# Kernel tuning notes

Hardware: AMD Instinct MI355X
Metric: run time of the kernel (lower is better)

## Reference

```python
import jax, jax.numpy as jnp
import numpy as np

B = 32768   # batch
T = 10      # n_track
NW = 3      # n_waypoints
D = 128     # d_model
H = 8       # num_heads
HD = D // H # head_dim = 16


def _ln(x, g, b, eps=1e-5):
    m = jnp.mean(x, axis=-1, keepdims=True)
    v = jnp.mean((x - m) ** 2, axis=-1, keepdims=True)
    return (x - m) * jax.lax.rsqrt(v + eps) * g + b


def setup_inputs() -> dict:
    key = jax.random.key(0)
    ks = jax.random.split(key, 16)
    rn = lambda k, shape, s=0.05: jax.random.normal(k, shape, dtype=jnp.float32) * s
    return {
        "track_left": jax.random.normal(ks[0], (B, T, 2), dtype=jnp.float32),
        "track_right": jax.random.normal(ks[1], (B, T, 2), dtype=jnp.float32),
        "coord_w": rn(ks[2], (D, 2), 0.5), "coord_b": jnp.zeros((D,), jnp.float32),
        "pos_emb": rn(ks[3], (T, D), 0.02),
        "side_emb": rn(ks[4], (2, D), 0.02),
        "query_emb": rn(ks[5], (NW, D), 0.02),
        "tokens_ln_g": jnp.ones((D,), jnp.float32), "tokens_ln_b": jnp.zeros((D,), jnp.float32),
        "queries_ln_g": jnp.ones((D,), jnp.float32), "queries_ln_b": jnp.zeros((D,), jnp.float32),
        "in_proj_w": rn(ks[6], (3 * D, D)), "in_proj_b": jnp.zeros((3 * D,), jnp.float32),
        "out_proj_w": rn(ks[7], (D, D)), "out_proj_b": jnp.zeros((D,), jnp.float32),
        "fc1_w": rn(ks[8], (2 * D, D)), "fc1_b": jnp.zeros((2 * D,), jnp.float32),
        "fc2_w": rn(ks[9], (D, 2 * D)), "fc2_b": jnp.zeros((D,), jnp.float32),
        "post_attn_ln_g": jnp.ones((D,), jnp.float32), "post_attn_ln_b": jnp.zeros((D,), jnp.float32),
        "post_ffn_ln_g": jnp.ones((D,), jnp.float32), "post_ffn_ln_b": jnp.zeros((D,), jnp.float32),
        "head_w": rn(ks[10], (2, D)), "head_b": jnp.zeros((2,), jnp.float32),
    }


def reference(track_left, track_right, coord_w, coord_b, pos_emb, side_emb,
              query_emb, tokens_ln_g, tokens_ln_b, queries_ln_g, queries_ln_b,
              in_proj_w, in_proj_b, out_proj_w, out_proj_b, fc1_w, fc1_b,
              fc2_w, fc2_b, post_attn_ln_g, post_attn_ln_b, post_ffn_ln_g,
              post_ffn_ln_b, head_w, head_b):
    # --- tokens: embed + add pos/side + LN ---  (dropout = eval-mode identity)
    coords = jnp.concatenate([track_left, track_right], axis=1)       # [B, 2T, 2]
    coord_feat = coords @ coord_w.T + coord_b                          # [B, 2T, D]
    pos_vecs = jnp.concatenate([pos_emb, pos_emb], axis=0)             # [2T, D]
    side_vecs = jnp.concatenate([
        jnp.broadcast_to(side_emb[0], (T, D)),
        jnp.broadcast_to(side_emb[1], (T, D))], axis=0)                # [2T, D]
    tokens = _ln(coord_feat + pos_vecs + side_vecs, tokens_ln_g, tokens_ln_b)  # [B, 2T, D]

    # --- queries (shared across batch) ---
    queries = _ln(query_emb, queries_ln_g, queries_ln_b)               # [NW, D]

    # --- MHA (batch_first, packed qkv in_proj as in nn.MultiheadAttention) ---
    wq, wk, wv = in_proj_w[:D], in_proj_w[D:2 * D], in_proj_w[2 * D:]
    bq, bk, bv = in_proj_b[:D], in_proj_b[D:2 * D], in_proj_b[2 * D:]
    q = (queries @ wq.T + bq).reshape(NW, H, HD)                       # [NW, H, HD]
    k = (tokens @ wk.T + bk).reshape(-1, 2 * T, H, HD)                 # [B, 2T, H, HD]
    v = (tokens @ wv.T + bv).reshape(-1, 2 * T, H, HD)                 # [B, 2T, H, HD]
    scores = jnp.einsum('whd,bkhd->bhwk', q, k) / jnp.sqrt(jnp.float32(HD))
    attn = jax.nn.softmax(scores, axis=-1)                             # [B, H, NW, 2T]
    ctx = jnp.einsum('bhwk,bkhd->bwhd', attn, v).reshape(-1, NW, D)    # [B, NW, D]
    attn_out = ctx @ out_proj_w.T + out_proj_b                         # [B, NW, D]

    # --- residual + LN + FFN + residual + LN + head ---
    x = _ln(queries[None, :, :] + attn_out, post_attn_ln_g, post_attn_ln_b)
    h = jax.nn.relu(x @ fc1_w.T + fc1_b)
    h = h @ fc2_w.T + fc2_b
    x = _ln(x + h, post_ffn_ln_g, post_ffn_ln_b)
    return x @ head_w.T + head_b                                       # [B, NW, 2]
```

## Files before the change

### kernel.cpp

```cpp
#include <hip/hip_runtime.h>
#include <hip/hip_bf16.h>


typedef __bf16 bf16x8 __attribute__((ext_vector_type(8)));
typedef float  f32x4  __attribute__((ext_vector_type(4)));
static_assert(sizeof(bf16x8) == 16, "bf16x8 must be 16B");

__device__ __forceinline__ unsigned short f2b(float x) {
  __bf16 h = (__bf16)x;
  return __builtin_bit_cast(unsigned short, h);
}
__device__ __forceinline__ float b2f(unsigned short u) {
  return (float)__builtin_bit_cast(__bf16, u);
}
__device__ __forceinline__ float dot4(float4 a, float4 b) {
  return a.x*b.x + a.y*b.y + a.z*b.z + a.w*b.w;
}
__device__ __forceinline__ f32x4 mfma16(bf16x8 a, bf16x8 b, f32x4 c) {
  return __builtin_amdgcn_mfma_f32_16x16x32_bf16(a, b, c, 0, 0, 0);
}

#define WS_OM    0
#define WS_FC1   49152
#define WS_FC2   114688
#define WS_QN    192000
#define WS_SB    193536
#define WS_SU    195456
#define WS_SCAL  195744
#define WS_SUB   195756
#define WS_SWB   195836
#define WS_SBB   195916

__device__ float mean128(float v, volatile float* red) {
  #pragma unroll
  for (int o = 32; o; o >>= 1) v += __shfl_down(v, o, 64);
  __syncthreads();
  if ((threadIdx.x & 63) == 0) red[threadIdx.x >> 6] = v;
  __syncthreads();
  return (red[0] + red[1]) * (1.0f / 128.0f);
}

__global__ void k_prep(
    const float* __restrict__ coord_w, const float* __restrict__ coord_b,
    const float* __restrict__ pos_emb, const float* __restrict__ side_emb,
    const float* __restrict__ query_emb,
    const float* __restrict__ tln_g, const float* __restrict__ tln_b,
    const float* __restrict__ qln_g, const float* __restrict__ qln_b,
    const float* __restrict__ ipw, const float* __restrict__ ipb,
    const float* __restrict__ opw, const float* __restrict__ opb,
    const float* __restrict__ f1w, const float* __restrict__ f2w,
    char* __restrict__ ws)
{
  const int b = blockIdx.x, tid = threadIdx.x;
  if (b >= 21) {
    if (b < 37) {
      unsigned short* dst = (unsigned short*)(ws + WS_FC1);
      int i0 = (b - 21)*2048;
      #pragma unroll
      for (int j = 0; j < 16; j++) { int i = i0 + j*128 + tid; dst[i] = f2b(f1w[i]); }
    } else {
      unsigned short* dst = (unsigned short*)(ws + WS_FC2);
      int i0 = (b - 37)*2048;
      #pragma unroll
      for (int j = 0; j < 16; j++) { int i = i0 + j*128 + tid; dst[i] = f2b(f2w[i]); }
    }
    return;
  }

  __shared__ float red[2];
  __shared__ float qn[3][128];
  __shared__ float qmat[3][128];
  __shared__ float vecA[128];
  __shared__ float vecB[128];
  __shared__ float vecC[128];
  __shared__ float kuA[128];
  __shared__ float kwA[128];
  __shared__ float kcA[128];
  const int d = tid;
  const int t = b;

  float u  = coord_w[d*2+0];
  float w2 = coord_w[d*2+1];
  float g  = tln_g[d];
  float mu = mean128(u,  red);
  float mw = mean128(w2, red);
  float uh = u - mu, wh = w2 - mw;

  #pragma unroll
  for (int w = 0; w < 3; w++) {
    float qe = query_emb[w*128 + d];
    float m  = mean128(qe, red);
    float m2 = mean128(qe*qe, red);
    float var = m2 - m*m;
    qn[w][d] = (qe - m) * rsqrtf(var + 1e-5f) * qln_g[d] + qln_b[d];
  }
  __syncthreads();
  {
    const float* wqr = ipw + d*128;
    float a0 = 0, a1 = 0, a2 = 0;
    for (int k4 = 0; k4 < 32; k4++) {
      float4 wv4 = *(const float4*)&wqr[k4*4];
      a0 += dot4(wv4, *(const float4*)&qn[0][k4*4]);
      a1 += dot4(wv4, *(const float4*)&qn[1][k4*4]);
      a2 += dot4(wv4, *(const float4*)&qn[2][k4*4]);
    }
    float bq = ipb[d];
    qmat[0][d] = a0 + bq; qmat[1][d] = a1 + bq; qmat[2][d] = a2 + bq;
  }
  __syncthreads();

  if (t < 20) {
    float base = coord_b[d] + pos_emb[(t % 10)*128 + d] + side_emb[(t < 10 ? 0 : 1)*128 + d];
    float mb = mean128(base, red);
    float bh = base - mb;
    float sub = mean128(uh*bh, red);
    float swb = mean128(wh*bh, red);
    float sbb = mean128(bh*bh, red);
    if (d == 0) {
      ((float*)(ws + WS_SUB))[t] = sub;
      ((float*)(ws + WS_SWB))[t] = swb;
      ((float*)(ws + WS_SBB))[t] = sbb;
    }
    vecA[d] = bh * g;
    __syncthreads();
    const float* wkr = ipw + (128 + d)*128;
    const float* wvr = ipw + (256 + d)*128;
    float kb = 0, vb = 0;
    for (int k4 = 0; k4 < 32; k4++) {
      float4 a4 = *(const float4*)&vecA[k4*4];
      kb += dot4(*(const float4*)&wkr[k4*4], a4);
      vb += dot4(*(const float4*)&wvr[k4*4], a4);
    }
    kuA[d] = kb;
    vecB[d] = vb;
    __syncthreads();
    if (d < 24) {
      int w = d / 8, h = d % 8;
      float s = 0;
      #pragma unroll
      for (int dl = 0; dl < 16; dl++) s += qmat[w][h*16 + dl] * kuA[h*16 + dl];
      ((float*)(ws + WS_SB))[(w*8 + h)*20 + t] = 0.25f * s;
    }
    {
      const float* opr = opw + d*128;
      float acc[8] = {0,0,0,0,0,0,0,0};
      #pragma unroll
      for (int k4 = 0; k4 < 32; k4++) {
        float4 o4 = *(const float4*)&opr[k4*4];
        acc[k4 >> 2] += dot4(o4, *(const float4*)&vecB[k4*4]);
      }
      unsigned short* OMr = (unsigned short*)(ws + WS_OM) + d*192;
      #pragma unroll
      for (int h = 0; h < 8; h++) OMr[h*20 + t] = f2b(acc[h]);
    }
  } else {
    float suu = mean128(uh*uh, red);
    float sww = mean128(wh*wh, red);
    float suw = mean128(uh*wh, red);
    if (d == 0) {
      float* sc = (float*)(ws + WS_SCAL);
      sc[0] = suu; sc[1] = sww; sc[2] = suw;
    }
    vecA[d] = uh * g; vecB[d] = wh * g; vecC[d] = tln_b[d];
    __syncthreads();
    const float* wkr = ipw + (128 + d)*128;
    const float* wvr = ipw + (256 + d)*128;
    float ku = 0, kw = 0, kc = 0, vu = 0, vw = 0, vc = 0;
    for (int k4 = 0; k4 < 32; k4++) {
      float4 a4 = *(const float4*)&vecA[k4*4];
      float4 b4 = *(const float4*)&vecB[k4*4];
      float4 c4 = *(const float4*)&vecC[k4*4];
      float4 kv = *(const float4*)&wkr[k4*4];
      float4 vv = *(const float4*)&wvr[k4*4];
      ku += dot4(kv, a4); kw += dot4(kv, b4); kc += dot4(kv, c4);
      vu += dot4(vv, a4); vw += dot4(vv, b4); vc += dot4(vv, c4);
    }
    kc += ipb[128 + d]; vc += ipb[256 + d];
    kuA[d] = ku; kwA[d] = kw; kcA[d] = kc;
    float* qnw = (float*)(ws + WS_QN);
    qnw[0*128 + d] = qn[0][d]; qnw[1*128 + d] = qn[1][d]; qnw[2*128 + d] = qn[2][d];
    __syncthreads();
    vecA[d] = vu; vecB[d] = vw; vecC[d] = vc;
    __syncthreads();
    if (d < 24) {
      int w = d / 8, h = d % 8;
      float su = 0, sw = 0, sc2 = 0;
      #pragma unroll
      for (int dl = 0; dl < 16; dl++) {
        float q = qmat[w][h*16 + dl];
        su  += q * kuA[h*16 + dl];
        sw  += q * kwA[h*16 + dl];
        sc2 += q * kcA[h*16 + dl];
      }
      float* o = (float*)(ws + WS_SU);
      o[ 0 + w*8 + h] = 0.25f * su;
      o[24 + w*8 + h] = 0.25f * sw;
      o[48 + w*8 + h] = 0.25f * sc2;
    }
    {
      const float* opr = opw + d*128;
      float au[8] = {0,0,0,0,0,0,0,0};
      float aw[8] = {0,0,0,0,0,0,0,0};
      float ac = 0;
      #pragma unroll
      for (int k4 = 0; k4 < 32; k4++) {
        float4 o4 = *(const float4*)&opr[k4*4];
        au[k4 >> 2] += dot4(o4, *(const float4*)&vecA[k4*4]);
        aw[k4 >> 2] += dot4(o4, *(const float4*)&vecB[k4*4]);
        ac          += dot4(o4, *(const float4*)&vecC[k4*4]);
      }
      unsigned short* OMr = (unsigned short*)(ws + WS_OM) + d*192;
      #pragma unroll
      for (int h = 0; h < 8; h++) {
        OMr[160 + h] = f2b(au[h]);
        OMr[168 + h] = f2b(aw[h]);
      }
      OMr[176] = f2b(ac + opb[d]);
      #pragma unroll
      for (int i = 177; i < 192; i++) OMr[i] = 0;
    }
  }
}

#define GE 16
#define MR 48
#define SMEM_SZ 32256

__global__ __launch_bounds__(256, 3) void k_main(
    const float* __restrict__ tl, const float* __restrict__ tr,
    const float* __restrict__ f1b, const float* __restrict__ f2b_,
    const float* __restrict__ pag, const float* __restrict__ pab,
    const float* __restrict__ pfg, const float* __restrict__ pfb,
    const float* __restrict__ hw, const float* __restrict__ hb,
    const char* __restrict__ ws, float* __restrict__ out)
{
  __shared__ __align__(16) char smem[SMEM_SZ];
  unsigned short* Z  = (unsigned short*)(smem);
  unsigned short* X  = (unsigned short*)(smem);
  float* Pp2  = (float*)(smem + 13056);
  float* msc2 = (float*)(smem + 14592);
  float* Op   = (float*)(smem + 14976);
  float* xr   = (float*)(smem + 19200);
  float* yr   = (float*)(smem + 20480);
  float* rsA  = (float*)(smem + 21760);
  float* Sbl  = (float*)(smem + 23040);
  float* SulA = (float*)(smem + 24960);
  float* QNl  = (float*)(smem + 25248);
  float* pagl = (float*)(smem + 26784);
  float* pabl = (float*)(smem + 27296);
  float* Pp   = (float*)(smem + 27808);
  float* mscA = (float*)(smem + 29344);
  unsigned short* h1 = (unsigned short*)(smem + 19200);

  const unsigned short* OM = (const unsigned short*)(ws + WS_OM);
  const unsigned short* W1 = (const unsigned short*)(ws + WS_FC1);
  const unsigned short* W2 = (const unsigned short*)(ws + WS_FC2);
  const float* QNw  = (const float*)(ws + WS_QN);
  const float* SBw  = (const float*)(ws + WS_SB);
  const float* SUw  = (const float*)(ws + WS_SU);
  const float* SCAL = (const float*)(ws + WS_SCAL);
  const float* SUB  = (const float*)(ws + WS_SUB);
  const float* SWB  = (const float*)(ws + WS_SWB);
  const float* SBB  = (const float*)(ws + WS_SBB);

  const int tid  = threadIdx.x;
  const int wg   = blockIdx.x;
  const int lane = tid & 63;
  const int wv   = tid >> 6;
  const int c    = lane & 15;
  const int g    = lane >> 4;
  const int nb   = wv * 32;

  for (int i = tid; i < 480; i += 256) Sbl[i] = SBw[i];
  if (tid < 72) SulA[tid] = SUw[tid];
  for (int i = tid; i < 384; i += 256) QNl[i] = QNw[i];
  if (tid < 128) { pagl[tid] = pag[tid]; pabl[tid] = pab[tid]; }
  if (tid < 48) {
    unsigned short* Zr = Z + tid*200;
    Zr[176] = 0x3F80;
    #pragma unroll
    for (int i = 177; i < 192; i++) Zr[i] = 0;
  }
  if (tid < 160) {
    int half = tid / 80;
    int i4   = tid % 80;
    const float* src = half ? tr : tl;
    float4 v = *(const float4*)(src + wg*(GE*20) + i4*4);
    int e  = i4 / 5;
    int j  = (i4 % 5) * 4;
    int t0 = half*10 + j/2;
    xr[e*20 + t0]     = v.x; yr[e*20 + t0]     = v.y;
    xr[e*20 + t0 + 1] = v.z; yr[e*20 + t0 + 1] = v.w;
  }
  __syncthreads();

  {
    float suu = SCAL[0], sww = SCAL[1], suw = SCAL[2];
    for (int i = tid; i < GE*20; i += 256) {
      int t = i % 20;
      float x = xr[i], y = yr[i];
      float var = suu*x*x + sww*y*y + 2.0f*suw*x*y
                + 2.0f*SUB[t]*x + 2.0f*SWB[t]*y + SBB[t];
      float rv = rsqrtf(var + 1e-5f);
      rsA[i] = rv; xr[i] = x*rv; yr[i] = y*rv;
    }
  }
  __syncthreads();

  if (tid < 128) {
    int e = tid >> 3, h = tid & 7;
    float xa[20], ya[20], ra[20];
    #pragma unroll
    for (int tb = 0; tb < 5; tb++) {
      float4 xv = *(const float4*)&xr[e*20 + tb*4];
      float4 yv = *(const float4*)&yr[e*20 + tb*4];
      float4 rv = *(const float4*)&rsA[e*20 + tb*4];
      xa[tb*4+0]=xv.x; xa[tb*4+1]=xv.y; xa[tb*4+2]=xv.z; xa[tb*4+3]=xv.w;
      ya[tb*4+0]=yv.x; ya[tb*4+1]=yv.y; ya[tb*4+2]=yv.z; ya[tb*4+3]=yv.w;
      ra[tb*4+0]=rv.x; ra[tb*4+1]=rv.y; ra[tb*4+2]=rv.z; ra[tb*4+3]=rv.w;
    }
    float s[3][20];
    #pragma unroll
    for (int w = 0; w < 3; w++) {
      float suv = SulA[w*8 + h], swv = SulA[24 + w*8 + h], scv = SulA[48 + w*8 + h];
      const float* sb = &Sbl[(w*8 + h)*20];
      #pragma unroll
      for (int tb = 0; tb < 5; tb++) {
        float4 s4 = *(const float4*)&sb[tb*4];
        s[w][tb*4+0] = fmaf(xa[tb*4+0],suv, fmaf(ya[tb*4+0],swv, fmaf(ra[tb*4+0],s4.x, scv)));
        s[w][tb*4+1] = fmaf(xa[tb*4+1],suv, fmaf(ya[tb*4+1],swv, fmaf(ra[tb*4+1],s4.y, scv)));
        s[w][tb*4+2] = fmaf(xa[tb*4+2],suv, fmaf(ya[tb*4+2],swv, fmaf(ra[tb*4+2],s4.z, scv)));
        s[w][tb*4+3] = fmaf(xa[tb*4+3],suv, fmaf(ya[tb*4+3],swv, fmaf(ra[tb*4+3],s4.w, scv)));
      }
    }
    unsigned short* Zr0 = Z + e*3*200;
    #pragma unroll
    for (int w = 0; w < 3; w++) {
      float m = s[w][0];
      #pragma unroll
      for (int t2 = 1; t2 < 20; t2++) m = fmaxf(m, s[w][t2]);
      float sum = 0;
      #pragma unroll
      for (int t2 = 0; t2 < 20; t2++) { float p = __expf(s[w][t2] - m); s[w][t2] = p; sum += p; }
      float inv = 1.0f / sum;
      float P = 0, Q = 0;
      #pragma unroll
      for (int t2 = 0; t2 < 20; t2++) { P = fmaf(s[w][t2], xa[t2], P); Q = fmaf(s[w][t2], ya[t2], Q); }
      P *= inv; Q *= inv;
      unsigned short* Zr = Zr0 + w*200;
      #pragma unroll
      for (int t2 = 0; t2 < 10; t2++) {
        unsigned int lo = f2b(s[w][2*t2]   * ra[2*t2]   * inv);
        unsigned int hi = f2b(s[w][2*t2+1] * ra[2*t2+1] * inv);
        *(unsigned int*)&Zr[h*20 + 2*t2] = lo | (hi << 16);
      }
      Zr[160 + h] = f2b(P);
      Zr[168 + h] = f2b(Q);
    }
  }
  __syncthreads();

  {
    bf16x8 Bf[2][6];
    #pragma unroll
    for (int nt = 0; nt < 2; nt++)
      #pragma unroll
      for (int kt = 0; kt < 6; kt++)
        Bf[nt][kt] = *(const bf16x8*)(OM + (nb + nt*16 + c)*192 + kt*32 + g*8);
    f32x4 acc[3][2];
    #pragma unroll
    for (int mt = 0; mt < 3; mt++)
      #pragma unroll
      for (int nt = 0; nt < 2; nt++) acc[mt][nt] = (f32x4){0.f,0.f,0.f,0.f};
    #pragma unroll
    for (int kt = 0; kt < 6; kt++) {
      bf16x8 Af[3];
      #pragma unroll
      for (int mt = 0; mt < 3; mt++)
        Af[mt] = *(const bf16x8*)(Z + (mt*16 + c)*200 + kt*32 + g*8);
      #pragma unroll
      for (int mt = 0; mt < 3; mt++)
        #pragma unroll
        for (int nt = 0; nt < 2; nt++)
          acc[mt][nt] = mfma16(Af[mt], Bf[nt][kt], acc[mt][nt]);
    }
    float p1[3][4], p2[3][4];
    #pragma unroll
    for (int mt = 0; mt < 3; mt++)
      #pragma unroll
      for (int j = 0; j < 4; j++) {
        int row = mt*16 + g*4 + j;
        int w = row % 3;
        float v0 = acc[mt][0][j] + QNl[w*128 + nb + c];
        float v1 = acc[mt][1][j] + QNl[w*128 + nb + 16 + c];
        acc[mt][0][j] = v0; acc[mt][1][j] = v1;
        p1[mt][j] = v0 + v1;
        p2[mt][j] = v0*v0 + v1*v1;
      }
    #pragma unroll
    for (int mt = 0; mt < 3; mt++)
      #pragma unroll
      for (int j = 0; j < 4; j++) {
        #pragma unroll
        for (int mk = 1; mk <= 8; mk <<= 1) {
          p1[mt][j] += __shfl_xor(p1[mt][j], mk, 64);
          p2[mt][j] += __shfl_xor(p2[mt][j], mk, 64);
        }
      }
    if (c < 4) {
      #pragma unroll
      for (int mt = 0; mt < 3; mt++) {
        float a = (c==0)?p1[mt][0]:(c==1)?p1[mt][1]:(c==2)?p1[mt][2]:p1[mt][3];
        float b = (c==0)?p2[mt][0]:(c==1)?p2[mt][1]:(c==2)?p2[mt][2]:p2[mt][3];
        int row = mt*16 + g*4 + c;
        *(float2*)&Pp[row*8 + wv*2] = make_float2(a, b);
      }
    }
    __syncthreads();
    if (tid < 192) {
      int row = tid >> 2, q = tid & 3;
      float2 pp = *(const float2*)&Pp[row*8 + q*2];
      float s1v = pp.x, s2v = pp.y;
      s1v += __shfl_xor(s1v, 1, 64); s1v += __shfl_xor(s1v, 2, 64);
      s2v += __shfl_xor(s2v, 1, 64); s2v += __shfl_xor(s2v, 2, 64);
      if (q == 0) {
        float m = s1v * (1.0f/128.0f);
        float var = s2v * (1.0f/128.0f) - m*m;
        *(float2*)&mscA[row*2] = make_float2(m, rsqrtf(var + 1e-5f));
      }
    }
    __syncthreads();
    {
      float pg0 = pagl[nb + c],      pb0 = pabl[nb + c];
      float pg1 = pagl[nb + 16 + c], pb1 = pabl[nb + 16 + c];
      #pragma unroll
      for (int mt = 0; mt < 3; mt++)
        #pragma unroll
        for (int j = 0; j < 4; j++) {
          int row = mt*16 + g*4 + j;
          float2 ms = *(const float2*)&mscA[row*2];
          X[row*136 + nb + c]      = f2b((acc[mt][0][j] - ms.x)*ms.y*pg0 + pb0);
          X[row*136 + nb + 16 + c] = f2b((acc[mt][1][j] - ms.x)*ms.y*pg1 + pb1);
        }
    }
  }
  __syncthreads();

  f32x4 acc2[3][2];
  #pragma unroll
  for (int mt = 0; mt < 3; mt++)
    #pragma unroll
    for (int nt = 0; nt < 2; nt++) acc2[mt][nt] = (f32x4){0.f,0.f,0.f,0.f};

  #pragma unroll
  for (int h = 0; h < 2; h++) {
    {
      bf16x8 Bf[2][4];
      #pragma unroll
      for (int nt = 0; nt < 2; nt++)
        #pragma unroll
        for (int kt = 0; kt < 4; kt++)
          Bf[nt][kt] = *(const bf16x8*)(W1 + (h*128 + nb + nt*16 + c)*128 + kt*32 + g*8);
      f32x4 acc[3][2];
      #pragma unroll
      for (int mt = 0; mt < 3; mt++)
        #pragma unroll
        for (int nt = 0; nt < 2; nt++) acc[mt][nt] = (f32x4){0.f,0.f,0.f,0.f};
      #pragma unroll
      for (int kt = 0; kt < 4; kt++) {
        bf16x8 Af[3];
        #pragma unroll
        for (int mt = 0; mt < 3; mt++)
          Af[mt] = *(const bf16x8*)(X + (mt*16 + c)*136 + kt*32 + g*8);
        #pragma unroll
        for (int mt = 0; mt < 3; mt++)
          #pragma unroll
          for (int nt = 0; nt < 2; nt++)
            acc[mt][nt] = mfma16(Af[mt], Bf[nt][kt], acc[mt][nt]);
      }
      float bb0 = f1b[h*128 + nb + c];
      float bb1 = f1b[h*128 + nb + 16 + c];
      #pragma unroll
      for (int mt = 0; mt < 3; mt++)
        #pragma unroll
        for (int j = 0; j < 4; j++) {
          int row = mt*16 + g*4 + j;
          h1[row*136 + nb + c]      = f2b(fmaxf(acc[mt][0][j] + bb0, 0.0f));
          h1[row*136 + nb + 16 + c] = f2b(fmaxf(acc[mt][1][j] + bb1, 0.0f));
        }
    }
    __syncthreads();
    {
      bf16x8 Bf[2][4];
      #pragma unroll
      for (int nt = 0; nt < 2; nt++)
        #pragma unroll
        for (int kt = 0; kt < 4; kt++)
          Bf[nt][kt] = *(const bf16x8*)(W2 + (nb + nt*16 + c)*256 + h*128 + kt*32 + g*8);
      #pragma unroll
      for (int kt = 0; kt < 4; kt++) {
        bf16x8 Af[3];
        #pragma unroll
        for (int mt = 0; mt < 3; mt++)
          Af[mt] = *(const bf16x8*)(h1 + (mt*16 + c)*136 + kt*32 + g*8);
        #pragma unroll
        for (int mt = 0; mt < 3; mt++)
          #pragma unroll
          for (int nt = 0; nt < 2; nt++)
            acc2[mt][nt] = mfma16(Af[mt], Bf[nt][kt], acc2[mt][nt]);
      }
    }
    if (h == 0) __syncthreads();
  }

  {
    float bb0 = f2b_[nb + c];
    float bb1 = f2b_[nb + 16 + c];
    float p1[3][4], p2[3][4];
    #pragma unroll
    for (int mt = 0; mt < 3; mt++)
      #pragma unroll
      for (int j = 0; j < 4; j++) {
        int row = mt*16 + g*4 + j;
        float v0 = acc2[mt][0][j] + bb0 + b2f(X[row*136 + nb + c]);
        float v1 = acc2[mt][1][j] + bb1 + b2f(X[row*136 + nb + 16 + c]);
        acc2[mt][0][j] = v0; acc2[mt][1][j] = v1;
        p1[mt][j] = v0 + v1;
        p2[mt][j] = v0*v0 + v1*v1;
      }
    #pragma unroll
    for (int mt = 0; mt < 3; mt++)
      #pragma unroll
      for (int j = 0; j < 4; j++) {
        #pragma unroll
        for (int mk = 1; mk <= 8; mk <<= 1) {
          p1[mt][j] += __shfl_xor(p1[mt][j], mk, 64);
          p2[mt][j] += __shfl_xor(p2[mt][j], mk, 64);
        }
      }
    if (c < 4) {
      #pragma unroll
      for (int mt = 0; mt < 3; mt++) {
        float a = (c==0)?p1[mt][0]:(c==1)?p1[mt][1]:(c==2)?p1[mt][2]:p1[mt][3];
        float b = (c==0)?p2[mt][0]:(c==1)?p2[mt][1]:(c==2)?p2[mt][2]:p2[mt][3];
        int row = mt*16 + g*4 + c;
        *(float2*)&Pp2[row*8 + wv*2] = make_float2(a, b);
      }
    }
    __syncthreads();
    if (tid < 192) {
      int row = tid >> 2, q = tid & 3;
      float2 pp = *(const float2*)&Pp2[row*8 + q*2];
      float s1v = pp.x, s2v = pp.y;
      s1v += __shfl_xor(s1v, 1, 64); s1v += __shfl_xor(s1v, 2, 64);
      s2v += __shfl_xor(s2v, 1, 64); s2v += __shfl_xor(s2v, 2, 64);
      if (q == 0) {
        float m = s1v * (1.0f/128.0f);
        float var = s2v * (1.0f/128.0f) - m*m;
        *(float2*)&msc2[row*2] = make_float2(m, rsqrtf(var + 1e-5f));
      }
    }
    __syncthreads();
    {
      float fg0 = pfg[nb + c],        fb0 = pfb[nb + c];
      float fg1 = pfg[nb + 16 + c],   fb1 = pfb[nb + 16 + c];
      float hw00 = hw[nb + c],        hw01 = hw[nb + 16 + c];
      float hw10 = hw[128 + nb + c],  hw11 = hw[128 + nb + 16 + c];
      float o0[3][4], o1[3][4];
      #pragma unroll
      for (int mt = 0; mt < 3; mt++)
        #pragma unroll
        for (int j = 0; j < 4; j++) {
          int row = mt*16 + g*4 + j;
          float2 ms = *(const float2*)&msc2[row*2];
          float x0 = (acc2[mt][0][j] - ms.x)*ms.y*fg0 + fb0;
          float x1 = (acc2[mt][1][j] - ms.x)*ms.y*fg1 + fb1;
          o0[mt][j] = x0*hw00 + x1*hw01;
          o1[mt][j] = x0*hw10 + x1*hw11;
        }
      #pragma unroll
      for (int mt = 0; mt < 3; mt++)
        #pragma unroll
        for (int j = 0; j < 4; j++) {
          #pragma unroll
          for (int mk = 1; mk <= 8; mk <<= 1) {
            o0[mt][j] += __shfl_xor(o0[mt][j], mk, 64);
            o1[mt][j] += __shfl_xor(o1[mt][j], mk, 64);
          }
        }
      if (c < 4) {
        #pragma unroll
        for (int mt = 0; mt < 3; mt++) {
          float a = (c==0)?o0[mt][0]:(c==1)?o0[mt][1]:(c==2)?o0[mt][2]:o0[mt][3];
          float b = (c==0)?o1[mt][0]:(c==1)?o1[mt][1]:(c==2)?o1[mt][2]:o1[mt][3];
          int row = mt*16 + g*4 + c;
          *(float2*)&Op[row*8 + wv*2] = make_float2(a, b);
        }
      }
    }
    __syncthreads();
    if (tid < 48) {
      float4 a = *(const float4*)&Op[tid*8];
      float4 b = *(const float4*)&Op[tid*8 + 4];
      out[(wg*48 + tid)*2]     = a.x + a.z + b.x + b.z + hb[0];
      out[(wg*48 + tid)*2 + 1] = a.y + a.w + b.y + b.w + hb[1];
    }
  }
}

extern "C" void kernel_launch(void* const* d_in, const int* in_sizes, int n_in,
                              void* d_out, int out_size, void* d_ws, size_t ws_size,
                              hipStream_t stream) {
  const float* tl       = (const float*)d_in[0];
  const float* tr       = (const float*)d_in[1];
  const float* coord_w  = (const float*)d_in[2];
  const float* coord_b  = (const float*)d_in[3];
  const float* pos_emb  = (const float*)d_in[4];
  const float* side_emb = (const float*)d_in[5];
  const float* query_emb= (const float*)d_in[6];
  const float* tln_g    = (const float*)d_in[7];
  const float* tln_b    = (const float*)d_in[8];
  const float* qln_g    = (const float*)d_in[9];
  const float* qln_b    = (const float*)d_in[10];
  const float* ipw      = (const float*)d_in[11];
  const float* ipb      = (const float*)d_in[12];
  const float* opw      = (const float*)d_in[13];
  const float* opb      = (const float*)d_in[14];
  const float* f1w      = (const float*)d_in[15];
  const float* f1b      = (const float*)d_in[16];
  const float* f2w      = (const float*)d_in[17];
  const float* f2b2     = (const float*)d_in[18];
  const float* pag      = (const float*)d_in[19];
  const float* pab      = (const float*)d_in[20];
  const float* pfg      = (const float*)d_in[21];
  const float* pfb      = (const float*)d_in[22];
  const float* hw       = (const float*)d_in[23];
  const float* hb       = (const float*)d_in[24];
  char* ws = (char*)d_ws;

  k_prep<<<53, 128, 0, stream>>>(coord_w, coord_b, pos_emb, side_emb, query_emb,
                                 tln_g, tln_b, qln_g, qln_b, ipw, ipb,
                                 opw, opb, f1w, f2w, ws);
  k_main<<<32768 / GE, 256, 0, stream>>>(tl, tr, f1b, f2b2, pag, pab, pfg, pfb,
                                         hw, hb, ws, (float*)d_out);
}
```

Baseline: 192.7 us.

## Pre-swizzle weights into MFMA fragment layout and prefetch B fragments before barriers

The prep kernel now writes the out-projection, fc1 and fc2 bf16 weights in a fragment-tiled layout, so each lane loads a contiguous 16-byte chunk at lane*8 rather than doing strided row reads. The main kernel issues these weight fragment loads before the preceding __syncthreads, which hides their global latency behind the barrier and LDS work. Launch bounds rise from 3 to 4 blocks per SM to allow more occupancy. The cost is more live registers across barriers, which together with the tighter register limit could cause spills.

```diff
diff --git a/kernel.cpp b/kernel.cpp
--- a/kernel.cpp
+++ b/kernel.cpp
@@ -18,6 +18,16 @@
 }
 __device__ __forceinline__ f32x4 mfma16(bf16x8 a, bf16x8 b, f32x4 c) {
   return __builtin_amdgcn_mfma_f32_16x16x32_bf16(a, b, c, 0, 0, 0);
+}
+
+__device__ __forceinline__ int om_off(int n, int k) {
+  return (((n >> 4)*6 + (k >> 5))*64 + ((k >> 3) & 3)*16 + (n & 15))*8 + (k & 7);
+}
+__device__ __forceinline__ int w1_off(int n, int k) {
+  return (((n >> 4)*4 + (k >> 5))*64 + ((k >> 3) & 3)*16 + (n & 15))*8 + (k & 7);
+}
+__device__ __forceinline__ int w2_off(int n, int k) {
+  return (((n >> 4)*8 + (k >> 5))*64 + ((k >> 3) & 3)*16 + (n & 15))*8 + (k & 7);
 }
 
 #define WS_OM    0
@@ -57,12 +67,18 @@
       unsigned short* dst = (unsigned short*)(ws + WS_FC1);
       int i0 = (b - 21)*2048;
       #pragma unroll
-      for (int j = 0; j < 16; j++) { int i = i0 + j*128 + tid; dst[i] = f2b(f1w[i]); }
+      for (int j = 0; j < 16; j++) {
+        int i = i0 + j*128 + tid;
+        dst[w1_off(i >> 7, i & 127)] = f2b(f1w[i]);
+      }
     } else {
       unsigned short* dst = (unsigned short*)(ws + WS_FC2);
       int i0 = (b - 37)*2048;
       #pragma unroll
-      for (int j = 0; j < 16; j++) { int i = i0 + j*128 + tid; dst[i] = f2b(f2w[i]); }
+      for (int j = 0; j < 16; j++) {
+        int i = i0 + j*128 + tid;
+        dst[w2_off(i >> 8, i & 255)] = f2b(f2w[i]);
+      }
     }
     return;
   }
@@ -78,6 +94,7 @@
   __shared__ float kcA[128];
   const int d = tid;
   const int t = b;
+  unsigned short* OMw = (unsigned short*)(ws + WS_OM);
 
   float u  = coord_w[d*2+0];
   float w2 = coord_w[d*2+1];
@@ -149,9 +166,8 @@
         float4 o4 = *(const float4*)&opr[k4*4];
         acc[k4 >> 2] += dot4(o4, *(const float4*)&vecB[k4*4]);
       }
-      unsigned short* OMr = (unsigned short*)(ws + WS_OM) + d*192;
-      #pragma unroll
-      for (int h = 0; h < 8; h++) OMr[h*20 + t] = f2b(acc[h]);
+      #pragma unroll
+      for (int h = 0; h < 8; h++) OMw[om_off(d, h*20 + t)] = f2b(acc[h]);
     }
   } else {
     float suu = mean128(uh*uh, red);
@@ -209,15 +225,14 @@
         aw[k4 >> 2] += dot4(o4, *(const float4*)&vecB[k4*4]);
         ac          += dot4(o4, *(const float4*)&vecC[k4*4]);
       }
-      unsigned short* OMr = (unsigned short*)(ws + WS_OM) + d*192;
       #pragma unroll
       for (int h = 0; h < 8; h++) {
-        OMr[160 + h] = f2b(au[h]);
-        OMr[168 + h] = f2b(aw[h]);
-      }
-      OMr[176] = f2b(ac + opb[d]);
-      #pragma unroll
-      for (int i = 177; i < 192; i++) OMr[i] = 0;
+        OMw[om_off(d, 160 + h)] = f2b(au[h]);
+        OMw[om_off(d, 168 + h)] = f2b(aw[h]);
+      }
+      OMw[om_off(d, 176)] = f2b(ac + opb[d]);
+      #pragma unroll
+      for (int i = 177; i < 192; i++) OMw[om_off(d, i)] = 0;
     }
   }
 }
@@ -226,7 +241,7 @@
 #define MR 48
 #define SMEM_SZ 32256
 
-__global__ __launch_bounds__(256, 3) void k_main(
+__global__ __launch_bounds__(256, 4) void k_main(
     const float* __restrict__ tl, const float* __restrict__ tr,
     const float* __restrict__ f1b, const float* __restrict__ f2b_,
     const float* __restrict__ pag, const float* __restrict__ pab,
@@ -252,9 +267,9 @@
   float* mscA = (float*)(smem + 29344);
   unsigned short* h1 = (unsigned short*)(smem + 19200);
 
-  const unsigned short* OM = (const unsigned short*)(ws + WS_OM);
-  const unsigned short* W1 = (const unsigned short*)(ws + WS_FC1);
-  const unsigned short* W2 = (const unsigned short*)(ws + WS_FC2);
+  const unsigned short* OMf = (const unsigned short*)(ws + WS_OM);
+  const unsigned short* W1f = (const unsigned short*)(ws + WS_FC1);
+  const unsigned short* W2f = (const unsigned short*)(ws + WS_FC2);
   const float* QNw  = (const float*)(ws + WS_QN);
   const float* SBw  = (const float*)(ws + WS_SB);
   const float* SUw  = (const float*)(ws + WS_SU);
@@ -358,15 +373,15 @@
       Zr[168 + h] = f2b(Q);
     }
   }
+  bf16x8 BfOM[2][6];
+  #pragma unroll
+  for (int nt = 0; nt < 2; nt++)
+    #pragma unroll
+    for (int kt = 0; kt < 6; kt++)
+      BfOM[nt][kt] = *(const bf16x8*)(OMf + ((wv*2 + nt)*6 + kt)*512 + lane*8);
   __syncthreads();
 
   {
-    bf16x8 Bf[2][6];
-    #pragma unroll
-    for (int nt = 0; nt < 2; nt++)
-      #pragma unroll
-      for (int kt = 0; kt < 6; kt++)
-        Bf[nt][kt] = *(const bf16x8*)(OM + (nb + nt*16 + c)*192 + kt*32 + g*8);
     f32x4 acc[3][2];
     #pragma unroll
     for (int mt = 0; mt < 3; mt++)
@@ -382,7 +397,7 @@
       for (int mt = 0; mt < 3; mt++)
         #pragma unroll
         for (int nt = 0; nt < 2; nt++)
-          acc[mt][nt] = mfma16(Af[mt], Bf[nt][kt], acc[mt][nt]);
+          acc[mt][nt] = mfma16(Af[mt], BfOM[nt][kt], acc[mt][nt]);
     }
     float p1[3][4], p2[3][4];
     #pragma unroll
@@ -444,6 +459,12 @@
         }
     }
   }
+  bf16x8 BfW1[2][4];
+  #pragma unroll
+  for (int nt = 0; nt < 2; nt++)
+    #pragma unroll
+    for (int kt = 0; kt < 4; kt++)
+      BfW1[nt][kt] = *(const bf16x8*)(W1f + ((wv*2 + nt)*4 + kt)*512 + lane*8);
   __syncthreads();
 
   f32x4 acc2[3][2];
@@ -455,12 +476,6 @@
   #pragma unroll
   for (int h = 0; h < 2; h++) {
     {
-      bf16x8 Bf[2][4];
-      #pragma unroll
-      for (int nt = 0; nt < 2; nt++)
-        #pragma unroll
-        for (int kt = 0; kt < 4; kt++)
-          Bf[nt][kt] = *(const bf16x8*)(W1 + (h*128 + nb + nt*16 + c)*128 + kt*32 + g*8);
       f32x4 acc[3][2];
       #pragma unroll
       for (int mt = 0; mt < 3; mt++)
@@ -476,7 +491,7 @@
         for (int mt = 0; mt < 3; mt++)
           #pragma unroll
           for (int nt = 0; nt < 2; nt++)
-            acc[mt][nt] = mfma16(Af[mt], Bf[nt][kt], acc[mt][nt]);
+            acc[mt][nt] = mfma16(Af[mt], BfW1[nt][kt], acc[mt][nt]);
       }
       float bb0 = f1b[h*128 + nb + c];
       float bb1 = f1b[h*128 + nb + 16 + c];
@@ -489,28 +504,33 @@
           h1[row*136 + nb + 16 + c] = f2b(fmaxf(acc[mt][1][j] + bb1, 0.0f));
         }
     }
-    __syncthreads();
-    {
-      bf16x8 Bf[2][4];
+    bf16x8 BfW2[2][4];
+    #pragma unroll
+    for (int nt = 0; nt < 2; nt++)
+      #pragma unroll
+      for (int kt = 0; kt < 4; kt++)
+        BfW2[nt][kt] = *(const bf16x8*)(W2f + ((wv*2 + nt)*8 + h*4 + kt)*512 + lane*8);
+    __syncthreads();
+    #pragma unroll
+    for (int kt = 0; kt < 4; kt++) {
+      bf16x8 Af[3];
+      #pragma unroll
+      for (int mt = 0; mt < 3; mt++)
+        Af[mt] = *(const bf16x8*)(h1 + (mt*16 + c)*136 + kt*32 + g*8);
+      #pragma unroll
+      for (int mt = 0; mt < 3; mt++)
+        #pragma unroll
+        for (int nt = 0; nt < 2; nt++)
+          acc2[mt][nt] = mfma16(Af[mt], BfW2[nt][kt], acc2[mt][nt]);
+    }
+    if (h == 0) {
       #pragma unroll
       for (int nt = 0; nt < 2; nt++)
         #pragma unroll
         for (int kt = 0; kt < 4; kt++)
-          Bf[nt][kt] = *(const bf16x8*)(W2 + (nb + nt*16 + c)*256 + h*128 + kt*32 + g*8);
-      #pragma unroll
-      for (int kt = 0; kt < 4; kt++) {
-        bf16x8 Af[3];
-        #pragma unroll
-        for (int mt = 0; mt < 3; mt++)
-          Af[mt] = *(const bf16x8*)(h1 + (mt*16 + c)*136 + kt*32 + g*8);
-        #pragma unroll
-        for (int mt = 0; mt < 3; mt++)
-          #pragma unroll
-          for (int nt = 0; nt < 2; nt++)
-            acc2[mt][nt] = mfma16(Af[mt], Bf[nt][kt], acc2[mt][nt]);
-      }
-    }
-    if (h == 0) __syncthreads();
+          BfW1[nt][kt] = *(const bf16x8*)(W1f + ((8 + wv*2 + nt)*4 + kt)*512 + lane*8);
+      __syncthreads();
+    }
   }
 
   {
```

Result: faster. 173.7 us (-9.9%).
